# Kernel optimization log

Hardware: AMD Instinct MI355X
Metric: run time of the kernel (lower is better)

## Reference

```python
import jax, jax.numpy as jnp
import numpy as np

MARGIN = 0.2
NEG_SENTINEL = -1e30


def setup_inputs() -> dict:
    key = jax.random.key(0)
    k1, k2 = jax.random.split(key)
    batch_reprs = jax.random.normal(k1, (4096, 128), dtype=jnp.float32)
    batch_labels = jax.random.randint(k2, (4096,), 0, 512, dtype=jnp.int64 if jax.config.jax_enable_x64 else jnp.int32)
    return {"batch_reprs": batch_reprs, "batch_labels": batch_labels}


def _loss(batch_reprs, batch_labels):
    # class match matrix (self-similarity kept, as in original)
    match = (batch_labels[:, None] == batch_labels[None, :]).astype(batch_reprs.dtype)  # [B,B]

    # pairwise euclidean distance (squared=False), sim = -dist
    sq = jnp.sum(batch_reprs * batch_reprs, axis=1)
    d2 = jnp.maximum(sq[:, None] + sq[None, :] - 2.0 * (batch_reprs @ batch_reprs.T), 0.0)
    zero = (d2 == 0.0).astype(batch_reprs.dtype)
    dist = jnp.sqrt(d2 + zero * 1e-16) * (1.0 - zero)
    sim_hat = -dist + (1.0 - match) * MARGIN  # use_margin=True

    # rank positions via double argsort (descending)
    order = jnp.argsort(-sim_hat, axis=1)
    rank = jnp.argsort(order, axis=1).astype(sim_hat.dtype) + 1.0  # [B,B], 1-based ranks

    k = jnp.sum(match, axis=1, keepdims=True)                      # n_pos per row, [B,1]
    fp = (match < 1.0) & (rank <= k)                               # false positives
    fp_num = jnp.sum(fp, axis=1, keepdims=True).astype(sim_hat.dtype)
    fn = (match > 0.0) & (rank > k)                                # false negatives

    n = sim_hat.shape[1]
    # per-row top-(fp_num) false negatives by sim_hat, vectorized via masked sort
    fn_scores = jnp.where(fn, sim_hat, NEG_SENTINEL)
    idx = jnp.argsort(-fn_scores, axis=1)
    fn_sorted = jnp.take_along_axis(sim_hat, idx, axis=1)
    fn_ranks = jnp.take_along_axis(rank, idx, axis=1)
    fn_mask_sorted = jnp.take_along_axis(fn, idx, axis=1)
    sel = (jnp.arange(n)[None, :] < fp_num) & fn_mask_sorted       # top fp_num entries

    # weighted margins (rows with fp_num==0 contribute 0 automatically)
    fp_term = jnp.sum(jnp.where(fp, sim_hat * (0.5 + (k - rank + 1.0) / k * 0.5), 0.0))
    fn_term = jnp.sum(jnp.where(sel, fn_sorted * (0.5 + (fn_ranks - k) / (n - k) * 0.5), 0.0))
    return fp_term - fn_term


def reference(batch_reprs, batch_labels):
    return _loss(batch_reprs, batch_labels)
```

## Files before the change

kernel.cpp:

```cpp
#include <hip/hip_runtime.h>
#include <cstdint>
#include <cstddef>

#define B 4096
#define D 128
#define MARGIN_F 0.2f
#define CW 256
#define ROWS 16
#define SSTR 4104

typedef short bf16x8 __attribute__((ext_vector_type(8)));
typedef float f32x4 __attribute__((ext_vector_type(4)));
typedef uint32_t u32x4 __attribute__((ext_vector_type(4)));

__device__ __forceinline__ uint32_t xform_key(float f) {
    uint32_t u = __float_as_uint(f);
    return u ^ (uint32_t)((((int32_t)u) >> 31) | 0x80000000);
}
__device__ __forceinline__ float unxform16(uint32_t k16) {
    uint32_t u = k16 << 16;
    u = (u & 0x80000000u) ? (u ^ 0x80000000u) : ~u;
    return __uint_as_float(u);
}
__device__ __forceinline__ unsigned short f2bf(float f) {
    uint32_t u = __float_as_uint(f);
    return (unsigned short)((u + 0x7FFFu + ((u >> 16) & 1u)) >> 16);
}

__global__ __launch_bounds__(256) void prep_kernel(const float* __restrict__ R,
                                                   float* __restrict__ sq,
                                                   unsigned short* __restrict__ Rb,
                                                   float* __restrict__ out) {
    if (blockIdx.x == 0 && threadIdx.x == 0) out[0] = 0.0f;
    int wave = threadIdx.x >> 6;
    int lane = threadIdx.x & 63;
    int row  = blockIdx.x * 4 + wave;
    const float2* R2 = (const float2*)R + (size_t)row * (D / 2);
    float2 v = R2[lane];
    ushort2 o; o.x = f2bf(v.x); o.y = f2bf(v.y);
    *(ushort2*)(Rb + (size_t)row * D + lane * 2) = o;
    float s = v.x * v.x + v.y * v.y;
#pragma unroll
    for (int off = 32; off > 0; off >>= 1) s += __shfl_down(s, off);
    if (lane == 0) sq[row] = s;
}

__global__ __launch_bounds__(512) void fused_loss(const unsigned short* __restrict__ Rb,
                                                  const float* __restrict__ sq,
                                                  const int* __restrict__ labels,
                                                  float* __restrict__ out) {
    __shared__ unsigned short S[ROWS * SSTR];
    __shared__ uint32_t cand_c[ROWS][CW];
    __shared__ int cnt[ROWS];

    const int tid  = threadIdx.x;
    const int wid  = tid >> 6, lane = tid & 63;
    const int q    = lane >> 4, t = lane & 15;
    const int r0   = blockIdx.x * ROWS;

    if (tid < ROWS) cnt[tid] = 0;

    bf16x8 af[4];
    const unsigned short* baseA = Rb + (size_t)(r0 + t) * D + q * 8;
#pragma unroll
    for (int kq = 0; kq < 4; ++kq)
        af[kq] = *(const bf16x8*)(baseA + kq * 32);

    float sqa[4]; int la[4];
#pragma unroll
    for (int rr = 0; rr < 4; ++rr) {
        sqa[rr] = sq[r0 + q * 4 + rr];
        la[rr]  = labels[r0 + q * 4 + rr];
    }

    for (int i = 0; i < 32; ++i) {
        const int jt  = wid * 32 + i;
        const int col = jt * 16 + t;
        const unsigned short* baseB = Rb + (size_t)col * D + q * 8;
        bf16x8 bfr[4];
#pragma unroll
        for (int kq = 0; kq < 4; ++kq)
            bfr[kq] = *(const bf16x8*)(baseB + kq * 32);
        f32x4 acc = (f32x4)0.0f;
#pragma unroll
        for (int kq = 0; kq < 4; ++kq)
            acc = __builtin_amdgcn_mfma_f32_16x16x32_bf16(af[kq], bfr[kq], acc, 0, 0, 0);

        const float sqc = sq[col];
        const int   lc  = labels[col];
#pragma unroll
        for (int rr = 0; rr < 4; ++rr) {
            float g  = acc[rr];
            float d2 = fmaxf(sqa[rr] + sqc - 2.0f * g, 0.0f);
            float dist = (d2 > 0.0f) ? sqrtf(d2) : 0.0f;
            float s = -dist + ((la[rr] == lc) ? 0.0f : MARGIN_F);
            uint32_t key = xform_key(s);
            S[(q * 4 + rr) * SSTR + col] = (unsigned short)((key + 0x8000u) >> 16);
        }
    }
    __syncthreads();

    float facc = 0.0f;
    const int4* lv = (const int4*)labels;

    for (int rr2 = 0; rr2 < 2; ++rr2) {
        const int row  = wid * 2 + rr2;
        const int grow = r0 + row;
        const int li   = labels[grow];

        u32x4 kv[8];
#pragma unroll
        for (int qq = 0; qq < 8; ++qq)
            kv[qq] = *(u32x4*)(&S[row * SSTR + (qq * 64 + lane) * 8]);

        uint64_t mbits = 0;
        uint32_t t1 = 0, t2 = 0;
#pragma unroll
        for (int qq = 0; qq < 8; ++qq) {
            const int lb = (qq * 64 + lane) * 2;
            int4 la4 = lv[lb], lc4 = lv[lb + 1];
            uint32_t u[8] = {kv[qq].x & 0xFFFFu, kv[qq].x >> 16,
                             kv[qq].y & 0xFFFFu, kv[qq].y >> 16,
                             kv[qq].z & 0xFFFFu, kv[qq].z >> 16,
                             kv[qq].w & 0xFFFFu, kv[qq].w >> 16};
#pragma unroll
            for (int c = 0; c < 8; ++c) {
                uint32_t mn = min(t1, u[c]);
                t1 = max(t1, u[c]);
                t2 = max(t2, mn);
            }
            mbits |= (uint64_t)(la4.x == li) << (qq * 8 + 0);
            mbits |= (uint64_t)(la4.y == li) << (qq * 8 + 1);
            mbits |= (uint64_t)(la4.z == li) << (qq * 8 + 2);
            mbits |= (uint64_t)(la4.w == li) << (qq * 8 + 3);
            mbits |= (uint64_t)(lc4.x == li) << (qq * 8 + 4);
            mbits |= (uint64_t)(lc4.y == li) << (qq * 8 + 5);
            mbits |= (uint64_t)(lc4.z == li) << (qq * 8 + 6);
            mbits |= (uint64_t)(lc4.w == li) << (qq * 8 + 7);
        }

        int kloc = __popcll(mbits);
#pragma unroll
        for (int off = 32; off > 0; off >>= 1) kloc += __shfl_xor(kloc, off);
        const int k = kloc;
        const float kf = (float)k;

        const int kneed = min(k, 128);
        uint32_t T = 0;
#pragma unroll
        for (int b = 15; b >= 0; --b) {
            uint32_t g = T | (1u << b);
            int c = __popcll(__ballot(t1 >= g)) + __popcll(__ballot(t2 >= g));
            if (c >= kneed) T = g;
        }
        const uint32_t combT = T << 12;

#pragma unroll
        for (int qq = 0; qq < 8; ++qq) {
            uint32_t u[8] = {kv[qq].x & 0xFFFFu, kv[qq].x >> 16,
                             kv[qq].y & 0xFFFFu, kv[qq].y >> 16,
                             kv[qq].z & 0xFFFFu, kv[qq].z >> 16,
                             kv[qq].w & 0xFFFFu, kv[qq].w >> 16};
            int jb = (qq * 64 + lane) * 8;
#pragma unroll
            for (int c = 0; c < 8; ++c) {
                int e = qq * 8 + c;
                uint32_t m = (uint32_t)((mbits >> e) & 1);
                if (u[c] >= T || m) {
                    int p = atomicAdd(&cnt[row], 1);
                    if (p < CW)
                        cand_c[row][p] = (u[c] << 12) | (uint32_t)(4095 - (jb + c)) | (m << 31);
                }
            }
        }
        const int ncand = min(cnt[row], CW);

        for (int s = lane; s < ncand; s += 64) {
            uint32_t cs = cand_c[row][s];
            uint32_t comb = cs & 0x7FFFFFFFu;
            int m = (int)(cs >> 31);
            if (comb >= combT) {
                int c2 = 0;
                for (int c = 0; c < ncand; ++c)
                    c2 += ((cand_c[row][c] & 0x7FFFFFFFu) > comb) ? 1 : 0;
                int rank = 1 + c2;
                float v = unxform16(comb >> 12);
                if (!m && rank <= k)
                    facc += v * (0.5f + ((kf - (float)rank + 1.0f) / kf) * 0.5f);
                else if (m && rank > k)
                    facc -= v * (0.5f + (((float)rank - kf) / (float)(B - k)) * 0.5f);
            }
        }

        uint32_t p0 = 0xFFFFFFFFu, p1 = 0xFFFFFFFFu, p2 = 0xFFFFFFFFu, p3 = 0xFFFFFFFFu;
        int np = 0;
        for (int c = 0; c <= ncand; ++c) {
            bool flushit = (c == ncand);
            if (!flushit) {
                uint32_t cc_ = cand_c[row][c];
                if ((cc_ & 0x80000000u) && (cc_ & 0x7FFFFFFFu) < combT) {
                    uint32_t comb = cc_ & 0x7FFFFFFFu;
                    if (np == 0) p0 = comb; else if (np == 1) p1 = comb;
                    else if (np == 2) p2 = comb; else p3 = comb;
                    ++np;
                    flushit = (np == 4);
                }
            }
            if (flushit && np > 0) {
                int c0 = 0, c1 = 0, c2 = 0, c3 = 0;
#pragma unroll
                for (int qq = 0; qq < 8; ++qq) {
                    uint32_t u[8] = {kv[qq].x & 0xFFFFu, kv[qq].x >> 16,
                                     kv[qq].y & 0xFFFFu, kv[qq].y >> 16,
                                     kv[qq].z & 0xFFFFu, kv[qq].z >> 16,
                                     kv[qq].w & 0xFFFFu, kv[qq].w >> 16};
                    int jb = (qq * 64 + lane) * 8;
#pragma unroll
                    for (int cc = 0; cc < 8; ++cc) {
                        uint32_t comb_e = (u[cc] << 12) | (uint32_t)(4095 - (jb + cc));
                        c0 += (comb_e > p0) ? 1 : 0;
                        c1 += (comb_e > p1) ? 1 : 0;
                        c2 += (comb_e > p2) ? 1 : 0;
                        c3 += (comb_e > p3) ? 1 : 0;
                    }
                }
#pragma unroll
                for (int off = 32; off > 0; off >>= 1) {
                    c0 += __shfl_xor(c0, off); c1 += __shfl_xor(c1, off);
                    c2 += __shfl_xor(c2, off); c3 += __shfl_xor(c3, off);
                }
                if (lane == 0) {
                    int rk[4] = {1 + c0, 1 + c1, 1 + c2, 1 + c3};
                    uint32_t pp[4] = {p0, p1, p2, p3};
                    for (int ii = 0; ii < np; ++ii) {
                        float v = unxform16(pp[ii] >> 12);
                        facc -= v * (0.5f + (((float)rk[ii] - kf) / (float)(B - k)) * 0.5f);
                    }
                }
                p0 = p1 = p2 = p3 = 0xFFFFFFFFu;
                np = 0;
            }
        }
    }

#pragma unroll
    for (int off = 32; off > 0; off >>= 1) facc += __shfl_xor(facc, off);
    if (lane == 0) atomicAdd(out, facc);
}

extern "C" void kernel_launch(void* const* d_in, const int* in_sizes, int n_in,
                              void* d_out, int out_size, void* d_ws, size_t ws_size,
                              hipStream_t stream) {
    const float* R      = (const float*)d_in[0];
    const int*   labels = (const int*)d_in[1];
    float* out = (float*)d_out;

    float*          sq = (float*)d_ws;
    unsigned short* Rb = (unsigned short*)((char*)d_ws + 16 * 1024);

    hipLaunchKernelGGL(prep_kernel, dim3(B / 4), dim3(256), 0, stream, R, sq, Rb, out);
    hipLaunchKernelGGL(fused_loss, dim3(B / ROWS), dim3(512), 0, stream,
                       Rb, sq, labels, out);
}
```

Before: 135.0 us.

## Precompute label match bitmasks and use one-row-per-wave 1024-thread blocks

The prep kernel now also builds a per-label 64-bit bitmask table of which columns share each label. The loss kernel then loads one mask word per lane instead of reading and comparing all 4096 labels for every row. The loss kernel doubles its block size to 1024 threads, so each of 16 waves handles a single row in the ranking phase. The Gram phase processes two column tiles per iteration to overlap loads and MFMAs. This trades extra workspace and prep work, plus higher register pressure, for less redundant label traffic and more parallel waves per block.

```diff
diff --git a/kernel.cpp b/kernel.cpp
--- a/kernel.cpp
+++ b/kernel.cpp
@@ -28,8 +28,10 @@
 }
 
 __global__ __launch_bounds__(256) void prep_kernel(const float* __restrict__ R,
+                                                   const int* __restrict__ labels,
                                                    float* __restrict__ sq,
                                                    unsigned short* __restrict__ Rb,
+                                                   unsigned long long* __restrict__ mask64,
                                                    float* __restrict__ out) {
     if (blockIdx.x == 0 && threadIdx.x == 0) out[0] = 0.0f;
     int wave = threadIdx.x >> 6;
@@ -43,12 +45,28 @@
 #pragma unroll
     for (int off = 32; off > 0; off >>= 1) s += __shfl_down(s, off);
     if (lane == 0) sq[row] = s;
-}
-
-__global__ __launch_bounds__(512) void fused_loss(const unsigned short* __restrict__ Rb,
-                                                  const float* __restrict__ sq,
-                                                  const int* __restrict__ labels,
-                                                  float* __restrict__ out) {
+
+    if (threadIdx.x < 32) {
+        int p  = blockIdx.x * 32 + threadIdx.x;
+        int l  = p >> 6;
+        int ln = p & 63;
+        unsigned long long m = 0ull;
+#pragma unroll
+        for (int qq = 0; qq < 8; ++qq) {
+            int jb = qq * 512 + ln * 8;
+#pragma unroll
+            for (int c = 0; c < 8; ++c)
+                m |= (unsigned long long)(labels[jb + c] == l) << (qq * 8 + c);
+        }
+        mask64[(size_t)l * 64 + ln] = m;
+    }
+}
+
+__global__ __launch_bounds__(1024, 4) void fused_loss(const unsigned short* __restrict__ Rb,
+                                                      const float* __restrict__ sq,
+                                                      const int* __restrict__ labels,
+                                                      const unsigned long long* __restrict__ mask64,
+                                                      float* __restrict__ out) {
     __shared__ unsigned short S[ROWS * SSTR];
     __shared__ uint32_t cand_c[ROWS][CW];
     __shared__ int cnt[ROWS];
@@ -73,52 +91,59 @@
         la[rr]  = labels[r0 + q * 4 + rr];
     }
 
-    for (int i = 0; i < 32; ++i) {
-        const int jt  = wid * 32 + i;
-        const int col = jt * 16 + t;
-        const unsigned short* baseB = Rb + (size_t)col * D + q * 8;
-        bf16x8 bfr[4];
+    for (int i = 0; i < 16; i += 2) {
+        const int col0 = (wid * 16 + i) * 16 + t;
+        const int col1 = col0 + 16;
+        const unsigned short* b0 = Rb + (size_t)col0 * D + q * 8;
+        const unsigned short* b1 = Rb + (size_t)col1 * D + q * 8;
+        bf16x8 f0[4], f1[4];
+#pragma unroll
+        for (int kq = 0; kq < 4; ++kq) f0[kq] = *(const bf16x8*)(b0 + kq * 32);
+#pragma unroll
+        for (int kq = 0; kq < 4; ++kq) f1[kq] = *(const bf16x8*)(b1 + kq * 32);
+        const float sqc0 = sq[col0], sqc1 = sq[col1];
+        const int   lc0  = labels[col0], lc1 = labels[col1];
+
+        f32x4 a0 = (f32x4)0.0f, a1 = (f32x4)0.0f;
 #pragma unroll
         for (int kq = 0; kq < 4; ++kq)
-            bfr[kq] = *(const bf16x8*)(baseB + kq * 32);
-        f32x4 acc = (f32x4)0.0f;
+            a0 = __builtin_amdgcn_mfma_f32_16x16x32_bf16(af[kq], f0[kq], a0, 0, 0, 0);
 #pragma unroll
         for (int kq = 0; kq < 4; ++kq)
-            acc = __builtin_amdgcn_mfma_f32_16x16x32_bf16(af[kq], bfr[kq], acc, 0, 0, 0);
-
-        const float sqc = sq[col];
-        const int   lc  = labels[col];
+            a1 = __builtin_amdgcn_mfma_f32_16x16x32_bf16(af[kq], f1[kq], a1, 0, 0, 0);
+
 #pragma unroll
         for (int rr = 0; rr < 4; ++rr) {
-            float g  = acc[rr];
-            float d2 = fmaxf(sqa[rr] + sqc - 2.0f * g, 0.0f);
-            float dist = (d2 > 0.0f) ? sqrtf(d2) : 0.0f;
-            float s = -dist + ((la[rr] == lc) ? 0.0f : MARGIN_F);
-            uint32_t key = xform_key(s);
-            S[(q * 4 + rr) * SSTR + col] = (unsigned short)((key + 0x8000u) >> 16);
+            float d20 = fmaxf(sqa[rr] + sqc0 - 2.0f * a0[rr], 0.0f);
+            float di0 = (d20 > 0.0f) ? sqrtf(d20) : 0.0f;
+            float s0 = -di0 + ((la[rr] == lc0) ? 0.0f : MARGIN_F);
+            S[(q * 4 + rr) * SSTR + col0] =
+                (unsigned short)((xform_key(s0) + 0x8000u) >> 16);
+            float d21 = fmaxf(sqa[rr] + sqc1 - 2.0f * a1[rr], 0.0f);
+            float di1 = (d21 > 0.0f) ? sqrtf(d21) : 0.0f;
+            float s1 = -di1 + ((la[rr] == lc1) ? 0.0f : MARGIN_F);
+            S[(q * 4 + rr) * SSTR + col1] =
+                (unsigned short)((xform_key(s1) + 0x8000u) >> 16);
         }
     }
     __syncthreads();
 
     float facc = 0.0f;
-    const int4* lv = (const int4*)labels;
-
-    for (int rr2 = 0; rr2 < 2; ++rr2) {
-        const int row  = wid * 2 + rr2;
+    {
+        const int row  = wid;
         const int grow = r0 + row;
         const int li   = labels[grow];
 
+        const uint64_t mbits = mask64[(size_t)li * 64 + lane];
+
         u32x4 kv[8];
 #pragma unroll
         for (int qq = 0; qq < 8; ++qq)
             kv[qq] = *(u32x4*)(&S[row * SSTR + (qq * 64 + lane) * 8]);
 
-        uint64_t mbits = 0;
         uint32_t t1 = 0, t2 = 0;
 #pragma unroll
         for (int qq = 0; qq < 8; ++qq) {
-            const int lb = (qq * 64 + lane) * 2;
-            int4 la4 = lv[lb], lc4 = lv[lb + 1];
             uint32_t u[8] = {kv[qq].x & 0xFFFFu, kv[qq].x >> 16,
                              kv[qq].y & 0xFFFFu, kv[qq].y >> 16,
                              kv[qq].z & 0xFFFFu, kv[qq].z >> 16,
@@ -129,14 +154,6 @@
                 t1 = max(t1, u[c]);
                 t2 = max(t2, mn);
             }
-            mbits |= (uint64_t)(la4.x == li) << (qq * 8 + 0);
-            mbits |= (uint64_t)(la4.y == li) << (qq * 8 + 1);
-            mbits |= (uint64_t)(la4.z == li) << (qq * 8 + 2);
-            mbits |= (uint64_t)(la4.w == li) << (qq * 8 + 3);
-            mbits |= (uint64_t)(lc4.x == li) << (qq * 8 + 4);
-            mbits |= (uint64_t)(lc4.y == li) << (qq * 8 + 5);
-            mbits |= (uint64_t)(lc4.z == li) << (qq * 8 + 6);
-            mbits |= (uint64_t)(lc4.w == li) << (qq * 8 + 7);
         }
 
         int kloc = __popcll(mbits);
@@ -255,10 +272,12 @@
     const int*   labels = (const int*)d_in[1];
     float* out = (float*)d_out;
 
-    float*          sq = (float*)d_ws;
-    unsigned short* Rb = (unsigned short*)((char*)d_ws + 16 * 1024);
-
-    hipLaunchKernelGGL(prep_kernel, dim3(B / 4), dim3(256), 0, stream, R, sq, Rb, out);
-    hipLaunchKernelGGL(fused_loss, dim3(B / ROWS), dim3(512), 0, stream,
-                       Rb, sq, labels, out);
-}
+    float*              sq   = (float*)d_ws;
+    unsigned short*     Rb   = (unsigned short*)((char*)d_ws + 16 * 1024);
+    unsigned long long* mask = (unsigned long long*)((char*)d_ws + 16 * 1024 + 1024 * 1024);
+
+    hipLaunchKernelGGL(prep_kernel, dim3(B / 4), dim3(256), 0, stream,
+                       R, labels, sq, Rb, mask, out);
+    hipLaunchKernelGGL(fused_loss, dim3(B / ROWS), dim3(1024), 0, stream,
+                       Rb, sq, labels, mask, out);
+}
```

Result: slower. 149.2 us (+10.5%).
